# Optimization experiments

Hardware: AMD Instinct MI355X
Metric: run time of the kernel (lower is better)

Reference implementation:

```python
import jax, jax.numpy as jnp
import numpy as np

B, T, C = 64, 256, 384
H = 6
D = C // H  # head_size = 64


def setup_inputs() -> dict:
    key = jax.random.key(0)
    ks = jax.random.split(key, 6)
    s = 1.0 / np.sqrt(C)
    return {
        "x": jax.random.normal(ks[0], (B, T, C), dtype=jnp.float32),
        "Wk": jax.random.uniform(ks[1], (C, C), jnp.float32, -s, s),
        "Wq": jax.random.uniform(ks[2], (C, C), jnp.float32, -s, s),
        "Wv": jax.random.uniform(ks[3], (C, C), jnp.float32, -s, s),
        "Wo": jax.random.uniform(ks[4], (C, C), jnp.float32, -s, s),
        "bo": jax.random.uniform(ks[5], (C,), jnp.float32, -s, s),
    }


def reference(x, Wk, Wq, Wv, Wo, bo):
    b, t, c = x.shape
    # QKV projections (no bias), split heads: [B, H, T, D]
    k = (x @ Wk.T).reshape(b, t, H, D).transpose(0, 2, 1, 3)
    q = (x @ Wq.T).reshape(b, t, H, D).transpose(0, 2, 1, 3)
    v = (x @ Wv.T).reshape(b, t, H, D).transpose(0, 2, 1, 3)
    # Scores scaled by C**-0.5 (as in the original module, not head_size**-0.5)
    wei = jnp.einsum("bhqd,bhkd->bhqk", q, k) * (c ** -0.5)
    mask = jnp.tril(jnp.ones((t, t), dtype=bool))
    wei = jnp.where(mask, wei, -jnp.inf)
    wei = jax.nn.softmax(wei, axis=-1)
    out = jnp.einsum("bhqk,bhkd->bhqd", wei, v)
    out = out.transpose(0, 2, 1, 3).reshape(b, t, c)
    # Output projection (dropout is identity at inference)
    return out @ Wo.T + bo
```

## Files before the change

### kernel.cpp

```cpp
#include <hip/hip_runtime.h>
#include <hip/hip_bf16.h>

typedef unsigned short u16;
typedef __attribute__((ext_vector_type(8))) short short8;
typedef __attribute__((ext_vector_type(4))) float f32x4;

#define BATCH 64
#define SEQ   256
#define CDIM  384
#define NHEAD 6
#define DHEAD 64
#define NROW  16384

constexpr float SCALE = 0.051031036307982884f;

__device__ __forceinline__ f32x4 mfma16(short8 a, short8 b, f32x4 c) {
    return __builtin_amdgcn_mfma_f32_16x16x32_bf16(a, b, c, 0, 0, 0);
}

__device__ __forceinline__ u16 f2b(float f) {
    __hip_bfloat16 h = __float2bfloat16(f);
    return *reinterpret_cast<u16*>(&h);
}

__device__ __forceinline__ void gload_lds16(const u16* g, u16* l) {
    __builtin_amdgcn_global_load_lds(
        (const __attribute__((address_space(1))) void*)g,
        (__attribute__((address_space(3))) void*)l, 16, 0, 0);
}

__global__ __launch_bounds__(256) void cvt_x(
        const float* __restrict__ s, u16* __restrict__ d)
{
    const int i = (blockIdx.x * 256 + threadIdx.x) * 8;
    const float4 a = *(const float4*)(s + i);
    const float4 b = *(const float4*)(s + i + 4);
    short8 r;
    r[0] = (short)f2b(a.x); r[1] = (short)f2b(a.y);
    r[2] = (short)f2b(a.z); r[3] = (short)f2b(a.w);
    r[4] = (short)f2b(b.x); r[5] = (short)f2b(b.y);
    r[6] = (short)f2b(b.z); r[7] = (short)f2b(b.w);
    *(short8*)(d + i) = r;
}

__global__ __launch_bounds__(256) void cvt_w(
        const float* __restrict__ w0, const float* __restrict__ w1,
        const float* __restrict__ w2, const float* __restrict__ w3,
        u16* __restrict__ d0, u16* __restrict__ d1,
        u16* __restrict__ d2, u16* __restrict__ d3)
{
    const int z = blockIdx.y;
    const float* s = (z == 0) ? w0 : (z == 1) ? w1 : (z == 2) ? w2 : w3;
    u16*         d = (z == 0) ? d0 : (z == 1) ? d1 : (z == 2) ? d2 : d3;
    const int i = (blockIdx.x * 256 + threadIdx.x) * 8;
    const float4 a = *(const float4*)(s + i);
    const float4 b = *(const float4*)(s + i + 4);
    short8 r;
    r[0] = (short)f2b(a.x); r[1] = (short)f2b(a.y);
    r[2] = (short)f2b(a.z); r[3] = (short)f2b(a.w);
    r[4] = (short)f2b(b.x); r[5] = (short)f2b(b.y);
    r[6] = (short)f2b(b.z); r[7] = (short)f2b(b.w);
    *(short8*)(d + i) = r;
}

__global__ __launch_bounds__(256) void gemm_qkv(
        const u16* __restrict__ X, const u16* __restrict__ Wk,
        const u16* __restrict__ Wv, const u16* __restrict__ Wq,
        u16* __restrict__ Kd, u16* __restrict__ VTd, u16* __restrict__ Qd)
{
    __shared__ u16 SMEM[17408];
    u16* As = SMEM;
    u16* Bs = SMEM + 4096;

    const int n0 = blockIdx.x * 128;
    const int m0 = blockIdx.y * 128;
    const int z  = blockIdx.z;
    const u16* W = (z == 0) ? Wk : (z == 1 ? Wv : Wq);

    const int tid  = threadIdx.x;
    const int lane = tid & 63;
    const int wv   = tid >> 6;
    const int l15  = lane & 15;
    const int q4   = lane >> 4;
    const int wm   = (wv >> 1) * 64;
    const int wn   = (wv & 1) * 64;

    f32x4 acc[4][4] = {};

    for (int kk = 0; kk < CDIM; kk += 32) {
        __syncthreads();
#pragma unroll
        for (int ch = 0; ch < 2; ++ch) {
            const int f = (ch * 256 + tid) * 8;
            const int r = f >> 5;
            const int c = f & 31;
            const int lb = (ch * 256 + wv * 64) * 8;
            gload_lds16(X + (size_t)(m0 + r) * CDIM + kk + c, As + lb);
            gload_lds16(W + (size_t)(n0 + r) * CDIM + kk + c, Bs + lb);
        }
        __syncthreads();

        short8 af[4], bf[4];
#pragma unroll
        for (int t = 0; t < 4; ++t) {
            af[t] = *(const short8*)(As + (wm + t * 16 + l15) * 32 + q4 * 8);
            bf[t] = *(const short8*)(Bs + (wn + t * 16 + l15) * 32 + q4 * 8);
        }
#pragma unroll
        for (int tm = 0; tm < 4; ++tm)
#pragma unroll
            for (int tn = 0; tn < 4; ++tn)
                acc[tm][tn] = mfma16(af[tm], bf[tn], acc[tm][tn]);
    }

    if (z != 1) {
        u16* D = (z == 0) ? Kd : Qd;
#pragma unroll
        for (int tm = 0; tm < 4; ++tm)
#pragma unroll
            for (int tn = 0; tn < 4; ++tn) {
                const int col = n0 + wn + tn * 16 + l15;
#pragma unroll
                for (int r = 0; r < 4; ++r) {
                    const int row = m0 + wm + tm * 16 + q4 * 4 + r;
                    const int b = row >> 8, t = row & 255;
                    const int h = col >> 6, d = col & 63;
                    D[(size_t)((b * NHEAD + h) * SEQ + t) * DHEAD + d] =
                        f2b(acc[tm][tn][r]);
                }
            }
    } else {
        __syncthreads();
        u16* T = SMEM;
#pragma unroll
        for (int tm = 0; tm < 4; ++tm)
#pragma unroll
            for (int tn = 0; tn < 4; ++tn) {
                const int cl = wn + tn * 16 + l15;
#pragma unroll
                for (int r = 0; r < 4; ++r) {
                    const int rl = wm + tm * 16 + q4 * 4 + r;
                    T[cl * 136 + rl] = f2b(acc[tm][tn][r]);
                }
            }
        __syncthreads();
        const int b  = m0 >> 8;
        const int t0 = m0 & 255;
        const int fl = tid >> 1;
        const int hf = tid & 1;
        const int fg = n0 + fl;
        const int h  = fg >> 6, d = fg & 63;
        u16* dst = VTd + ((size_t)(b * NHEAD + h) * DHEAD + d) * SEQ + t0 + hf * 64;
        const u16* src = T + fl * 136 + hf * 64;
#pragma unroll
        for (int j = 0; j < 8; ++j)
            *(uint4*)(dst + j * 8) = *(const uint4*)(src + j * 8);
    }
}

template <int CH>
__device__ __forceinline__ void attn_body(
        const u16* __restrict__ Qg, const u16* __restrict__ Kg,
        const u16* __restrict__ VTg, u16* __restrict__ Og, int bh,
        u16* SA, u16* Pbuf)
{
    constexpr int NKEY = 64 * (CH + 1);
    constexpr int KT   = NKEY / 16;
    constexpr int NPH  = (NKEY + 127) / 128;

    const int tid  = threadIdx.x;
    const int wv   = tid >> 6;
    const int lane = tid & 63;
    const int l15  = lane & 15;
    const int q4   = lane >> 4;
    const int qrow0 = CH * 64 + wv * 16;
    const int qmax  = qrow0 + 15;

    short8 aq[2];
#pragma unroll
    for (int ks = 0; ks < 2; ++ks)
        aq[ks] = *(const short8*)(Qg + (size_t)(bh * SEQ + qrow0 + l15) * DHEAD
                                     + ks * 32 + q4 * 8);

    u16* Kbuf = SA;
    f32x4 s[KT];
#pragma unroll
    for (int ph = 0; ph < NPH; ++ph) {
        const int rows = (NKEY - ph * 128) < 128 ? (NKEY - ph * 128) : 128;
        for (int it = 0; it < rows / 32; ++it) {
            const int r  = it * 32 + (tid >> 3);
            const int d0 = (tid & 7) * 8;
            *(uint4*)(Kbuf + r * 72 + d0) =
                *(const uint4*)(Kg + (size_t)(bh * SEQ + ph * 128 + r) * DHEAD + d0);
        }
        __syncthreads();
#pragma unroll
        for (int t = 0; t < rows / 16; ++t) {
            const int gt = ph * 8 + t;
            if (gt * 16 <= qmax) {
                f32x4 z = {0.f, 0.f, 0.f, 0.f};
#pragma unroll
                for (int ks = 0; ks < 2; ++ks) {
                    short8 bk = *(const short8*)(Kbuf + (t * 16 + l15) * 72
                                                 + ks * 32 + q4 * 8);
                    z = mfma16(aq[ks], bk, z);
                }
                const int kc = gt * 16 + l15;
#pragma unroll
                for (int r = 0; r < 4; ++r) {
                    float v = z[r] * SCALE;
                    if (kc > qrow0 + q4 * 4 + r) v = -1e30f;
                    z[r] = v;
                }
                s[gt] = z;
            } else {
                f32x4 neg = {-1e30f, -1e30f, -1e30f, -1e30f};
                s[gt] = neg;
            }
        }
        __syncthreads();
    }

    float mx[4], sm[4], rs[4];
#pragma unroll
    for (int r = 0; r < 4; ++r) {
        float m = -1e30f;
#pragma unroll
        for (int t = 0; t < KT; ++t) m = fmaxf(m, s[t][r]);
#pragma unroll
        for (int off = 1; off < 16; off <<= 1)
            m = fmaxf(m, __shfl_xor(m, off, 16));
        mx[r] = m;
        sm[r] = 0.f;
    }
#pragma unroll
    for (int t = 0; t < KT; ++t)
#pragma unroll
        for (int r = 0; r < 4; ++r) {
            float p = __expf(s[t][r] - mx[r]);
            s[t][r] = p;
            sm[r] += p;
        }
#pragma unroll
    for (int r = 0; r < 4; ++r) {
#pragma unroll
        for (int off = 1; off < 16; off <<= 1)
            sm[r] += __shfl_xor(sm[r], off, 16);
        rs[r] = 1.f / sm[r];
    }

    u16* Vt = SA;
    u16* Pw = Pbuf + wv * 16 * 40;
    f32x4 o[4] = {};
#pragma unroll
    for (int ph = 0; ph < NPH; ++ph) {
        const int rows = (NKEY - ph * 128) < 128 ? (NKEY - ph * 128) : 128;
        const int cpr  = rows >> 3;
#pragma unroll
        for (int it = 0; it < 4; ++it) {
            if (it < cpr / 4) {
                const int flat = it * 256 + tid;
                const int rd = flat / cpr;
                const int kc = (flat - rd * cpr) * 8;
                *(uint4*)(Vt + rd * 136 + kc) =
                    *(const uint4*)(VTg + ((size_t)bh * DHEAD + rd) * SEQ
                                        + ph * 128 + kc);
            }
        }
        __syncthreads();
#pragma unroll
        for (int ks = 0; ks < rows / 32; ++ks) {
            const int gks = ph * 4 + ks;
            if (gks * 32 <= qmax) {
#pragma unroll
                for (int tt = 0; tt < 2; ++tt) {
                    const int gt = gks * 2 + tt;
#pragma unroll
                    for (int r = 0; r < 4; ++r)
                        Pw[(q4 * 4 + r) * 40 + tt * 16 + l15] = f2b(s[gt][r]);
                }
                asm volatile("s_waitcnt lgkmcnt(0)" ::: "memory");
                short8 ap = *(const short8*)(Pw + l15 * 40 + q4 * 8);
#pragma unroll
                for (int tn = 0; tn < 4; ++tn) {
                    short8 bv = *(const short8*)(Vt + (tn * 16 + l15) * 136
                                                 + ks * 32 + q4 * 8);
                    o[tn] = mfma16(ap, bv, o[tn]);
                }
            }
        }
        __syncthreads();
    }

#pragma unroll
    for (int tn = 0; tn < 4; ++tn) {
        const int d = tn * 16 + l15;
#pragma unroll
        for (int r = 0; r < 4; ++r) {
            const int qr = qrow0 + q4 * 4 + r;
            Og[(size_t)(bh * SEQ + qr) * DHEAD + d] = f2b(o[tn][r] * rs[r]);
        }
    }
}

__global__ __launch_bounds__(256) void attn_kernel(
        const u16* __restrict__ Qg, const u16* __restrict__ Kg,
        const u16* __restrict__ VTg, u16* __restrict__ Og)
{
    __shared__ u16 SA[128 * 72];
    __shared__ u16 Pbuf[4 * 16 * 40];
    const int bh = blockIdx.y;
    switch (blockIdx.x) {
        case 0: attn_body<0>(Qg, Kg, VTg, Og, bh, SA, Pbuf); break;
        case 1: attn_body<1>(Qg, Kg, VTg, Og, bh, SA, Pbuf); break;
        case 2: attn_body<2>(Qg, Kg, VTg, Og, bh, SA, Pbuf); break;
        default: attn_body<3>(Qg, Kg, VTg, Og, bh, SA, Pbuf); break;
    }
}

__global__ __launch_bounds__(256) void gemm_out(
        const u16* __restrict__ O, const u16* __restrict__ Wo,
        const float* __restrict__ bias, float* __restrict__ out)
{
    __shared__ u16 As[128 * 32];
    __shared__ u16 Bs[128 * 32];

    const int n0 = blockIdx.x * 128;
    const int m0 = blockIdx.y * 128;

    const int tid  = threadIdx.x;
    const int lane = tid & 63;
    const int wv   = tid >> 6;
    const int l15  = lane & 15;
    const int q4   = lane >> 4;
    const int wm   = (wv >> 1) * 64;
    const int wn   = (wv & 1) * 64;

    f32x4 acc[4][4] = {};

    for (int kk = 0; kk < CDIM; kk += 32) {
        __syncthreads();
#pragma unroll
        for (int ch = 0; ch < 2; ++ch) {
            const int f = (ch * 256 + tid) * 8;
            const int r = f >> 5;
            const int c = f & 31;
            const int row = m0 + r;
            const int b = row >> 8, t = row & 255;
            const int k = kk + c;
            const int hh = k >> 6, dd = k & 63;
            const int lb = (ch * 256 + wv * 64) * 8;
            gload_lds16(O + (size_t)((b * NHEAD + hh) * SEQ + t) * DHEAD + dd,
                        As + lb);
            gload_lds16(Wo + (size_t)(n0 + r) * CDIM + kk + c, Bs + lb);
        }
        __syncthreads();

        short8 af[4], bf[4];
#pragma unroll
        for (int t = 0; t < 4; ++t) {
            af[t] = *(const short8*)(As + (wm + t * 16 + l15) * 32 + q4 * 8);
            bf[t] = *(const short8*)(Bs + (wn + t * 16 + l15) * 32 + q4 * 8);
        }
#pragma unroll
        for (int tm = 0; tm < 4; ++tm)
#pragma unroll
            for (int tn = 0; tn < 4; ++tn)
                acc[tm][tn] = mfma16(af[tm], bf[tn], acc[tm][tn]);
    }

#pragma unroll
    for (int tm = 0; tm < 4; ++tm) {
#pragma unroll
        for (int tn = 0; tn < 4; ++tn) {
            const int col = n0 + wn + tn * 16 + l15;
            const float bb = bias[col];
#pragma unroll
            for (int r = 0; r < 4; ++r) {
                const int row = m0 + wm + tm * 16 + q4 * 4 + r;
                out[(size_t)row * CDIM + col] = acc[tm][tn][r] + bb;
            }
        }
    }
}

extern "C" void kernel_launch(void* const* d_in, const int* in_sizes, int n_in,
                              void* d_out, int out_size, void* d_ws, size_t ws_size,
                              hipStream_t stream)
{
    const float* x  = (const float*)d_in[0];
    const float* Wk = (const float*)d_in[1];
    const float* Wq = (const float*)d_in[2];
    const float* Wv = (const float*)d_in[3];
    const float* Wo = (const float*)d_in[4];
    const float* bo = (const float*)d_in[5];
    float* out = (float*)d_out;

    const size_t SZ = (size_t)NROW * CDIM;
    const size_t WZ = (size_t)CDIM * CDIM;
    u16* xb  = (u16*)d_ws;
    u16* Wkb = xb  + SZ;
    u16* Wqb = Wkb + WZ;
    u16* Wvb = Wqb + WZ;
    u16* Wob = Wvb + WZ;
    u16* Kw  = Wob + WZ;
    u16* Qw  = Kw + SZ;
    u16* Ow  = Qw + SZ;
    u16* VTw = (u16*)d_out;

    cvt_x<<<dim3((int)(SZ / 2048)), 256, 0, stream>>>(x, xb);
    cvt_w<<<dim3((int)(WZ / 2048), 4), 256, 0, stream>>>(
        Wk, Wq, Wv, Wo, Wkb, Wqb, Wvb, Wob);

    dim3 g1(CDIM / 128, NROW / 128, 3);
    gemm_qkv<<<g1, 256, 0, stream>>>(xb, Wkb, Wvb, Wqb, Kw, VTw, Qw);

    dim3 g2(4, BATCH * NHEAD);
    attn_kernel<<<g2, 256, 0, stream>>>(Qw, Kw, VTw, Ow);

    dim3 g3(CDIM / 128, NROW / 128);
    gemm_out<<<g3, 256, 0, stream>>>(Ow, Wob, bo, out);
}
```

Before: 157.4 us.

## Fuse attention into online softmax, use register-staged GEMM loads, flatten QKV grid

```diff
diff --git a/kernel.cpp b/kernel.cpp
--- a/kernel.cpp
+++ b/kernel.cpp
@@ -21,12 +21,6 @@
 __device__ __forceinline__ u16 f2b(float f) {
     __hip_bfloat16 h = __float2bfloat16(f);
     return *reinterpret_cast<u16*>(&h);
-}
-
-__device__ __forceinline__ void gload_lds16(const u16* g, u16* l) {
-    __builtin_amdgcn_global_load_lds(
-        (const __attribute__((address_space(1))) void*)g,
-        (__attribute__((address_space(3))) void*)l, 16, 0, 0);
 }
 
 __global__ __launch_bounds__(256) void cvt_x(
@@ -72,9 +66,9 @@
     u16* As = SMEM;
     u16* Bs = SMEM + 4096;
 
-    const int n0 = blockIdx.x * 128;
+    const int n0 = (blockIdx.x % 3) * 128;
+    const int z  = blockIdx.x / 3;
     const int m0 = blockIdx.y * 128;
-    const int z  = blockIdx.z;
     const u16* W = (z == 0) ? Wk : (z == 1 ? Wv : Wq);
 
     const int tid  = threadIdx.x;
@@ -88,15 +82,21 @@
     f32x4 acc[4][4] = {};
 
     for (int kk = 0; kk < CDIM; kk += 32) {
-        __syncthreads();
+        short8 areg[2], breg[2];
 #pragma unroll
         for (int ch = 0; ch < 2; ++ch) {
             const int f = (ch * 256 + tid) * 8;
             const int r = f >> 5;
             const int c = f & 31;
-            const int lb = (ch * 256 + wv * 64) * 8;
-            gload_lds16(X + (size_t)(m0 + r) * CDIM + kk + c, As + lb);
-            gload_lds16(W + (size_t)(n0 + r) * CDIM + kk + c, Bs + lb);
+            areg[ch] = *(const short8*)(X + (size_t)(m0 + r) * CDIM + kk + c);
+            breg[ch] = *(const short8*)(W + (size_t)(n0 + r) * CDIM + kk + c);
+        }
+        __syncthreads();
+#pragma unroll
+        for (int ch = 0; ch < 2; ++ch) {
+            const int f = (ch * 256 + tid) * 8;
+            *(short8*)(As + f) = areg[ch];
+            *(short8*)(Bs + f) = breg[ch];
         }
         __syncthreads();
 
@@ -162,10 +162,9 @@
 __device__ __forceinline__ void attn_body(
         const u16* __restrict__ Qg, const u16* __restrict__ Kg,
         const u16* __restrict__ VTg, u16* __restrict__ Og, int bh,
-        u16* SA, u16* Pbuf)
+        u16* Kbuf , u16* Vt , u16* Pbuf )
 {
     constexpr int NKEY = 64 * (CH + 1);
-    constexpr int KT   = NKEY / 16;
     constexpr int NPH  = (NKEY + 127) / 128;
 
     const int tid  = threadIdx.x;
@@ -182,80 +181,26 @@
         aq[ks] = *(const short8*)(Qg + (size_t)(bh * SEQ + qrow0 + l15) * DHEAD
                                      + ks * 32 + q4 * 8);
 
-    u16* Kbuf = SA;
-    f32x4 s[KT];
+    float mrow[4], lrow[4];
+#pragma unroll
+    for (int r = 0; r < 4; ++r) { mrow[r] = -1e30f; lrow[r] = 0.f; }
+    f32x4 o[4] = {};
+    u16* Pw = Pbuf + wv * 16 * 40;
+
 #pragma unroll
     for (int ph = 0; ph < NPH; ++ph) {
         const int rows = (NKEY - ph * 128) < 128 ? (NKEY - ph * 128) : 128;
-        for (int it = 0; it < rows / 32; ++it) {
-            const int r  = it * 32 + (tid >> 3);
-            const int d0 = (tid & 7) * 8;
-            *(uint4*)(Kbuf + r * 72 + d0) =
-                *(const uint4*)(Kg + (size_t)(bh * SEQ + ph * 128 + r) * DHEAD + d0);
-        }
-        __syncthreads();
-#pragma unroll
-        for (int t = 0; t < rows / 16; ++t) {
-            const int gt = ph * 8 + t;
-            if (gt * 16 <= qmax) {
-                f32x4 z = {0.f, 0.f, 0.f, 0.f};
-#pragma unroll
-                for (int ks = 0; ks < 2; ++ks) {
-                    short8 bk = *(const short8*)(Kbuf + (t * 16 + l15) * 72
-                                                 + ks * 32 + q4 * 8);
-                    z = mfma16(aq[ks], bk, z);
-                }
-                const int kc = gt * 16 + l15;
-#pragma unroll
-                for (int r = 0; r < 4; ++r) {
-                    float v = z[r] * SCALE;
-                    if (kc > qrow0 + q4 * 4 + r) v = -1e30f;
-                    z[r] = v;
-                }
-                s[gt] = z;
-            } else {
-                f32x4 neg = {-1e30f, -1e30f, -1e30f, -1e30f};
-                s[gt] = neg;
-            }
-        }
-        __syncthreads();
-    }
-
-    float mx[4], sm[4], rs[4];
-#pragma unroll
-    for (int r = 0; r < 4; ++r) {
-        float m = -1e30f;
-#pragma unroll
-        for (int t = 0; t < KT; ++t) m = fmaxf(m, s[t][r]);
-#pragma unroll
-        for (int off = 1; off < 16; off <<= 1)
-            m = fmaxf(m, __shfl_xor(m, off, 16));
-        mx[r] = m;
-        sm[r] = 0.f;
-    }
-#pragma unroll
-    for (int t = 0; t < KT; ++t)
-#pragma unroll
-        for (int r = 0; r < 4; ++r) {
-            float p = __expf(s[t][r] - mx[r]);
-            s[t][r] = p;
-            sm[r] += p;
-        }
-#pragma unroll
-    for (int r = 0; r < 4; ++r) {
-#pragma unroll
-        for (int off = 1; off < 16; off <<= 1)
-            sm[r] += __shfl_xor(sm[r], off, 16);
-        rs[r] = 1.f / sm[r];
-    }
-
-    u16* Vt = SA;
-    u16* Pw = Pbuf + wv * 16 * 40;
-    f32x4 o[4] = {};
-#pragma unroll
-    for (int ph = 0; ph < NPH; ++ph) {
-        const int rows = (NKEY - ph * 128) < 128 ? (NKEY - ph * 128) : 128;
-        const int cpr  = rows >> 3;
+
+#pragma unroll
+        for (int it = 0; it < 4; ++it) {
+            if (it < rows / 32) {
+                const int r  = it * 32 + (tid >> 3);
+                const int d0 = (tid & 7) * 8;
+                *(uint4*)(Kbuf + r * 72 + d0) =
+                    *(const uint4*)(Kg + (size_t)(bh * SEQ + ph * 128 + r) * DHEAD + d0);
+            }
+        }
+        const int cpr = rows >> 3;
 #pragma unroll
         for (int it = 0; it < 4; ++it) {
             if (it < cpr / 4) {
@@ -268,30 +213,99 @@
             }
         }
         __syncthreads();
-#pragma unroll
-        for (int ks = 0; ks < rows / 32; ++ks) {
-            const int gks = ph * 4 + ks;
-            if (gks * 32 <= qmax) {
-#pragma unroll
-                for (int tt = 0; tt < 2; ++tt) {
-                    const int gt = gks * 2 + tt;
-#pragma unroll
-                    for (int r = 0; r < 4; ++r)
-                        Pw[(q4 * 4 + r) * 40 + tt * 16 + l15] = f2b(s[gt][r]);
+
+        f32x4 s[8];
+        const int ntiles = rows / 16;
+#pragma unroll
+        for (int t = 0; t < 8; ++t) {
+            if (t < ntiles) {
+                const int gt = ph * 8 + t;
+                if (gt * 16 <= qmax) {
+                    f32x4 zz = {0.f, 0.f, 0.f, 0.f};
+#pragma unroll
+                    for (int ks = 0; ks < 2; ++ks) {
+                        short8 bk = *(const short8*)(Kbuf + (t * 16 + l15) * 72
+                                                     + ks * 32 + q4 * 8);
+                        zz = mfma16(aq[ks], bk, zz);
+                    }
+                    const int kc = gt * 16 + l15;
+#pragma unroll
+                    for (int r = 0; r < 4; ++r) {
+                        float v = zz[r] * SCALE;
+                        if (kc > qrow0 + q4 * 4 + r) v = -1e30f;
+                        zz[r] = v;
+                    }
+                    s[t] = zz;
+                } else {
+                    f32x4 neg = {-1e30f, -1e30f, -1e30f, -1e30f};
+                    s[t] = neg;
                 }
-                asm volatile("s_waitcnt lgkmcnt(0)" ::: "memory");
-                short8 ap = *(const short8*)(Pw + l15 * 40 + q4 * 8);
-#pragma unroll
-                for (int tn = 0; tn < 4; ++tn) {
-                    short8 bv = *(const short8*)(Vt + (tn * 16 + l15) * 136
-                                                 + ks * 32 + q4 * 8);
-                    o[tn] = mfma16(ap, bv, o[tn]);
+            }
+        }
+
+#pragma unroll
+        for (int r = 0; r < 4; ++r) {
+            float pm = -1e30f;
+#pragma unroll
+            for (int t = 0; t < 8; ++t)
+                if (t < ntiles) pm = fmaxf(pm, s[t][r]);
+#pragma unroll
+            for (int off = 1; off < 16; off <<= 1)
+                pm = fmaxf(pm, __shfl_xor(pm, off, 16));
+            const float nm = fmaxf(mrow[r], pm);
+            const float alpha = __expf(mrow[r] - nm);
+            mrow[r] = nm;
+            lrow[r] *= alpha;
+#pragma unroll
+            for (int tn = 0; tn < 4; ++tn) o[tn][r] *= alpha;
+        }
+#pragma unroll
+        for (int t = 0; t < 8; ++t) {
+            if (t < ntiles) {
+#pragma unroll
+                for (int r = 0; r < 4; ++r) {
+                    const float p = __expf(s[t][r] - mrow[r]);
+                    s[t][r] = p;
+                    lrow[r] += p;
                 }
             }
         }
-        __syncthreads();
-    }
-
+
+#pragma unroll
+        for (int ks = 0; ks < 4; ++ks) {
+            if (ks < rows / 32) {
+                const int gks = ph * 4 + ks;
+                if (gks * 32 <= qmax) {
+#pragma unroll
+                    for (int tt = 0; tt < 2; ++tt) {
+#pragma unroll
+                        for (int r = 0; r < 4; ++r)
+                            Pw[(q4 * 4 + r) * 40 + tt * 16 + l15] =
+                                f2b(s[ks * 2 + tt][r]);
+                    }
+                    asm volatile("s_waitcnt lgkmcnt(0)" ::: "memory");
+                    short8 ap = *(const short8*)(Pw + l15 * 40 + q4 * 8);
+#pragma unroll
+                    for (int tn = 0; tn < 4; ++tn) {
+                        short8 bv = *(const short8*)(Vt + (tn * 16 + l15) * 136
+                                                     + ks * 32 + q4 * 8);
+                        o[tn] = mfma16(ap, bv, o[tn]);
+                    }
+                }
+            }
+        }
+        if (ph + 1 < NPH) __syncthreads();
+    }
+
+    float rs[4];
+#pragma unroll
+    for (int r = 0; r < 4; ++r) {
+        float l = lrow[r];
+#pragma unroll
+        for (int off = 1; off < 16; off <<= 1)
+            l += __shfl_xor(l, off, 16);
+        rs[r] = 1.f / l;
+    }
 #pragma unroll
     for (int tn = 0; tn < 4; ++tn) {
         const int d = tn * 16 + l15;
@@ -307,14 +321,15 @@
         const u16* __restrict__ Qg, const u16* __restrict__ Kg,
         const u16* __restrict__ VTg, u16* __restrict__ Og)
 {
-    __shared__ u16 SA[128 * 72];
+    __shared__ u16 Kbuf[128 * 72];
+    __shared__ u16 Vt[64 * 136];
     __shared__ u16 Pbuf[4 * 16 * 40];
     const int bh = blockIdx.y;
     switch (blockIdx.x) {
-        case 0: attn_body<0>(Qg, Kg, VTg, Og, bh, SA, Pbuf); break;
-        case 1: attn_body<1>(Qg, Kg, VTg, Og, bh, SA, Pbuf); break;
-        case 2: attn_body<2>(Qg, Kg, VTg, Og, bh, SA, Pbuf); break;
-        default: attn_body<3>(Qg, Kg, VTg, Og, bh, SA, Pbuf); break;
+        case 0: attn_body<0>(Qg, Kg, VTg, Og, bh, Kbuf, Vt, Pbuf); break;
+        case 1: attn_body<1>(Qg, Kg, VTg, Og, bh, Kbuf, Vt, Pbuf); break;
+        case 2: attn_body<2>(Qg, Kg, VTg, Og, bh, Kbuf, Vt, Pbuf); break;
+        default: attn_body<3>(Qg, Kg, VTg, Og, bh, Kbuf, Vt, Pbuf); break;
     }
 }
 
@@ -339,7 +354,8 @@
     f32x4 acc[4][4] = {};
 
     for (int kk = 0; kk < CDIM; kk += 32) {
-        __syncthreads();
+        uint4 areg[2];
+        short8 breg[2];
 #pragma unroll
         for (int ch = 0; ch < 2; ++ch) {
             const int f = (ch * 256 + tid) * 8;
@@ -349,10 +365,16 @@
             const int b = row >> 8, t = row & 255;
             const int k = kk + c;
             const int hh = k >> 6, dd = k & 63;
-            const int lb = (ch * 256 + wv * 64) * 8;
-            gload_lds16(O + (size_t)((b * NHEAD + hh) * SEQ + t) * DHEAD + dd,
-                        As + lb);
-            gload_lds16(Wo + (size_t)(n0 + r) * CDIM + kk + c, Bs + lb);
+            areg[ch] = *(const uint4*)(O +
+                (size_t)((b * NHEAD + hh) * SEQ + t) * DHEAD + dd);
+            breg[ch] = *(const short8*)(Wo + (size_t)(n0 + r) * CDIM + kk + c);
+        }
+        __syncthreads();
+#pragma unroll
+        for (int ch = 0; ch < 2; ++ch) {
+            const int f = (ch * 256 + tid) * 8;
+            *(uint4*)(As + f)  = areg[ch];
+            *(short8*)(Bs + f) = breg[ch];
         }
         __syncthreads();
 
@@ -412,7 +434,7 @@
     cvt_w<<<dim3((int)(WZ / 2048), 4), 256, 0, stream>>>(
         Wk, Wq, Wv, Wo, Wkb, Wqb, Wvb, Wob);
 
-    dim3 g1(CDIM / 128, NROW / 128, 3);
+    dim3 g1(9, NROW / 128);
     gemm_qkv<<<g1, 256, 0, stream>>>(xb, Wkb, Wvb, Wqb, Kw, VTw, Qw);
 
     dim3 g2(4, BATCH * NHEAD);
```

Result: slower. 168.4 us (+7.0%).
